# Performance work log

Hardware: AMD Instinct MI355X
Metric: run time of the kernel (lower is better)

Reference implementation:

```python
import jax, jax.numpy as jnp
import numpy as np

N_MIRNAS = 60000
N_DISEASES = 40000
N_NODES = N_MIRNAS + N_DISEASES
D = 64          # embedding_dim
L = 2           # n_layers
R = 8           # num_relations (hardcoded in module)
B = 4           # num_bases (hardcoded in module)
E = 2_000_000   # total edges


def setup_inputs() -> dict:
    key = jax.random.key(0)
    ks = jax.random.split(key, 7)
    node_embeddings = jax.random.normal(ks[0], (N_NODES, D), jnp.float32) * 0.1
    basis = jax.random.normal(ks[1], (L, B, D, D), jnp.float32) * 0.05   # basis_weights per layer
    coeff = jax.random.normal(ks[2], (L, R, B), jnp.float32) * 0.2       # relation coefficients
    self_w = jax.random.normal(ks[3], (L, D, D), jnp.float32) * 0.05     # self-loop linear (no bias)
    bias = jnp.zeros((L, D), jnp.float32)
    edge_index = jax.random.randint(ks[4], (2, E), 0, N_NODES, dtype=jnp.int32)
    edge_type = jax.random.randint(ks[5], (E,), 0, R, dtype=jnp.int32)
    return dict(node_embeddings=node_embeddings, basis=basis, coeff=coeff,
                self_w=self_w, bias=bias, edge_index=edge_index, edge_type=edge_type)


def _rgcn_layer(x, basis, coeff, self_w, bias, edge_index, edge_type):
    # weight_r = sum_b coeff[r,b] * basis[b]  (same as torch.einsum('rb,bio->rio'))
    n = x.shape[0]
    W = jnp.einsum('rb,bio->rio', coeff, basis)            # [R, D, D]
    # transform all nodes under every relation once, then gather per edge:
    # equivalent to per-relation mask -> gather -> mm -> index_add in the original
    h = jnp.einsum('ni,rio->rno', x, W)                    # [R, N, D]
    msgs = h[edge_type, edge_index[0]]                     # [E, D] = x[src] @ W[edge_type]
    agg = jax.ops.segment_sum(msgs, edge_index[1], num_segments=n)  # index_add_ scatter
    out = x @ self_w + agg + bias                          # self-loop + messages + bias
    # dropout is identity in eval mode; module applies ReLU last
    return jax.nn.relu(out)


def reference(node_embeddings, basis, coeff, self_w, bias, edge_index, edge_type):
    x = node_embeddings
    for l in range(L):
        x = _rgcn_layer(x, basis[l], coeff[l], self_w[l], bias[l], edge_index, edge_type)
    return x[:N_MIRNAS], x[N_MIRNAS:]
```

## Files before the change

kernel.cpp:

```cpp
#include <hip/hip_runtime.h>
#include <hip/hip_bf16.h>

#define DD 64
#define EPB 8192
#define WPAD 72

typedef unsigned int u32;
typedef __attribute__((ext_vector_type(8))) short bf16x8;
typedef __attribute__((ext_vector_type(8))) unsigned short u16x8;
typedef __attribute__((ext_vector_type(4))) float f32x4;

__device__ __forceinline__ float bf2f(unsigned short u) {
  union { u32 i; float f; } c;
  c.i = ((u32)u) << 16;
  return c.f;
}
__device__ __forceinline__ unsigned short f2bf(float f) {
  __hip_bfloat16 h = __float2bfloat16(f);
  return *reinterpret_cast<unsigned short*>(&h);
}


__global__ __launch_bounds__(256) void zero_u32_kernel(u32* __restrict__ p, int n) {
  int i = blockIdx.x * 256 + threadIdx.x;
  if (i < n) p[i] = 0u;
}

__global__ __launch_bounds__(256) void coarse_hist_kernel(
    const int* __restrict__ edst, u32* __restrict__ ccnt,
    int E, int sh_bin, int nbins) {
  __shared__ u32 lh[256];
  const int t = threadIdx.x;
  for (int j = t; j < nbins; j += 256) lh[j] = 0u;
  __syncthreads();
  for (int e = blockIdx.x * 256 + t; e < E; e += gridDim.x * 256)
    atomicAdd(&lh[edst[e] >> sh_bin], 1u);
  __syncthreads();
  for (int j = t; j < nbins; j += 256) {
    u32 c = lh[j];
    if (c) atomicAdd(&ccnt[j], c);
  }
}

__global__ __launch_bounds__(256) void coarse_scan_kernel(
    const u32* __restrict__ ccnt, u32* __restrict__ bin_base,
    u32* __restrict__ bin_cursor, int nbins, int E) {
  __shared__ u32 s[256];
  const int t = threadIdx.x;
  u32 v = (t < nbins) ? ccnt[t] : 0u;
  s[t] = v;
  __syncthreads();
  for (int off = 1; off < 256; off <<= 1) {
    u32 x = (t >= off) ? s[t - off] : 0u;
    __syncthreads();
    s[t] += x;
    __syncthreads();
  }
  if (t < nbins) {
    u32 ex = s[t] - v;
    bin_base[t] = ex;
    bin_cursor[t] = ex;
  }
  if (t == 0) bin_base[nbins] = (u32)E;
}

__global__ __launch_bounds__(256) void binscatter_kernel(
    const int* __restrict__ esrc, const int* __restrict__ edst,
    const int* __restrict__ et, u32* __restrict__ bin_cursor,
    u32* __restrict__ tmp, int E, int sh_bin, int sh, int nbins) {
  __shared__ u32 lhist[256];
  __shared__ u32 lbase[256];
  const int t = threadIdx.x;
  const int base = blockIdx.x * EPB;
  for (int j = t; j < nbins; j += 256) lhist[j] = 0u;
  __syncthreads();
  u32 br[32];
#pragma unroll
  for (int k = 0; k < 32; ++k) {
    int e = base + k * 256 + t;
    if (e < E) {
      int bn = edst[e] >> sh_bin;
      u32 r = atomicAdd(&lhist[bn], 1u);
      br[k] = ((u32)bn << 13) | r;
    }
  }
  __syncthreads();
  for (int j = t; j < nbins; j += 256) {
    u32 c = lhist[j];
    lbase[j] = c ? atomicAdd(&bin_cursor[j], c) : 0u;
  }
  __syncthreads();
  const u32 wmask = (1u << sh_bin) - 1u;
#pragma unroll
  for (int k = 0; k < 32; ++k) {
    int e = base + k * 256 + t;
    if (e < E) {
      u32 bn = br[k] >> 13, r = br[k] & 0x1FFFu;
      u32 pos = lbase[bn] + r;
      u32 dlow = (u32)edst[e] & wmask;
      tmp[pos] = (u32)esrc[e] | ((u32)et[e] << sh) | (dlow << (sh + 3));
    }
  }
}

__global__ __launch_bounds__(1024) void finescatter_kernel(
    const u32* __restrict__ tmp, const u32* __restrict__ bin_base,
    u32* __restrict__ row_ptr, u32* __restrict__ packed,
    int N, int E, int sh_bin, int sh) {
  __shared__ u32 dcnt[1024];
  __shared__ u32 s[1024];
  const int t = threadIdx.x;
  const int b = blockIdx.x;
  const u32 beg = bin_base[b], end = bin_base[b + 1];
  const int W  = 1 << sh_bin;
  const int d0 = b << sh_bin;
  const int dsh = sh + 3;
  const u32 smask = (1u << sh) - 1u;

  if (t < W) dcnt[t] = 0u;
  __syncthreads();
  for (u32 e = beg + t; e < end; e += 1024)
    atomicAdd(&dcnt[tmp[e] >> dsh], 1u);
  __syncthreads();
  u32 v = (t < W) ? dcnt[t] : 0u;
  s[t] = v;
  __syncthreads();
  for (int off = 1; off < 1024; off <<= 1) {
    u32 x = (t >= off) ? s[t - off] : 0u;
    __syncthreads();
    s[t] += x;
    __syncthreads();
  }
  const u32 ex = s[t] - v;
  if (t < W) {
    int d = d0 + t;
    if (d < N) row_ptr[d] = beg + ex;
    dcnt[t] = beg + ex;
  }
  if (b == 0 && t == 0) row_ptr[N] = (u32)E;
  __syncthreads();
  for (u32 e = beg + t; e < end; e += 1024) {
    u32 p = tmp[e];
    u32 pos = atomicAdd(&dcnt[p >> dsh], 1u);
    u32 src = p & smask;
    u32 ty  = (p >> sh) & 7u;
    packed[pos] = ty * (u32)N + src;
  }
}


__global__ __launch_bounds__(256) void compute_wt_kernel(
    const float* __restrict__ basis, const float* __restrict__ coeff,
    const float* __restrict__ self_w, unsigned short* __restrict__ Wt16,
    int R, int Bn) {
  int idx = blockIdx.x * 256 + threadIdx.x;
  int total = (R + 1) * DD * DD;
  if (idx >= total) return;
  int m = idx >> 12;
  int k = (idx >> 6) & 63;
  int o = idx & 63;
  float acc = 0.f;
  if (m == R) {
    acc = self_w[k * DD + o];
  } else {
    for (int b = 0; b < Bn; ++b)
      acc += coeff[m * Bn + b] * basis[((size_t)b * DD + k) * DD + o];
  }
  Wt16[((size_t)m * DD + o) * DD + k] = f2bf(acc);
}

__global__ __launch_bounds__(256) void transform_h_kernel(
    const float* __restrict__ x, const unsigned short* __restrict__ Wt16,
    unsigned short* __restrict__ h16, int N, int R) {
  __shared__ unsigned short Ws[2][64 * WPAD];
  const int t    = threadIdx.x;
  const int w    = t >> 6;
  const int lane = t & 63;
  const int l16  = lane & 15;
  const int kg   = lane >> 4;
  const int node = blockIdx.x * DD + w * 16 + l16;
  const bool ok  = (node < N);

  bf16x8 Xfrag[2];
  {
    const float* xp = x + (size_t)(ok ? node : 0) * DD + kg * 8;
#pragma unroll
    for (int kc = 0; kc < 2; ++kc) {
      float4 v0 = ok ? *reinterpret_cast<const float4*>(xp + kc * 32)
                     : make_float4(0.f, 0.f, 0.f, 0.f);
      float4 v1 = ok ? *reinterpret_cast<const float4*>(xp + kc * 32 + 4)
                     : make_float4(0.f, 0.f, 0.f, 0.f);
      bf16x8 a;
      a[0] = (short)f2bf(v0.x); a[1] = (short)f2bf(v0.y);
      a[2] = (short)f2bf(v0.z); a[3] = (short)f2bf(v0.w);
      a[4] = (short)f2bf(v1.x); a[5] = (short)f2bf(v1.y);
      a[6] = (short)f2bf(v1.z); a[7] = (short)f2bf(v1.w);
      Xfrag[kc] = a;
    }
  }

  {
#pragma unroll
    for (int i = 0; i < 2; ++i) {
      int q = t + (i << 8);
      int row = q >> 3, c8 = (q & 7) << 3;
      u16x8 v = *reinterpret_cast<const u16x8*>(Wt16 + row * DD + c8);
      *reinterpret_cast<u16x8*>(&Ws[0][row * WPAD + c8]) = v;
    }
  }
  __syncthreads();

  for (int m = 0; m <= R; ++m) {
    const int cur = m & 1;
    if (m < R) {
      const unsigned short* wb = Wt16 + ((size_t)(m + 1) << 12);
#pragma unroll
      for (int i = 0; i < 2; ++i) {
        int q = t + (i << 8);
        int row = q >> 3, c8 = (q & 7) << 3;
        u16x8 v = *reinterpret_cast<const u16x8*>(wb + row * DD + c8);
        *reinterpret_cast<u16x8*>(&Ws[cur ^ 1][row * WPAD + c8]) = v;
      }
    }

    unsigned short* hp = h16 + (((size_t)m * N + node) << 6);
#pragma unroll
    for (int t4 = 0; t4 < 4; ++t4) {
      const unsigned short* ap = &Ws[cur][(t4 * 16 + l16) * WPAD + kg * 8];
      bf16x8 A0 = *reinterpret_cast<const bf16x8*>(ap);
      bf16x8 A1 = *reinterpret_cast<const bf16x8*>(ap + 32);
      f32x4 acc;
      acc[0] = 0.f; acc[1] = 0.f; acc[2] = 0.f; acc[3] = 0.f;
      acc = __builtin_amdgcn_mfma_f32_16x16x32_bf16(A0, Xfrag[0], acc, 0, 0, 0);
      acc = __builtin_amdgcn_mfma_f32_16x16x32_bf16(A1, Xfrag[1], acc, 0, 0, 0);
      if (ok) {
        ushort4 o4;
        o4.x = f2bf(acc[0]); o4.y = f2bf(acc[1]);
        o4.z = f2bf(acc[2]); o4.w = f2bf(acc[3]);
        *reinterpret_cast<ushort4*>(hp + t4 * 16 + kg * 4) = o4;
      }
    }
    __syncthreads();
  }
}

__global__ __launch_bounds__(256) void aggregate_out_kernel(
    const u32* __restrict__ packed, const u32* __restrict__ row_ptr,
    const unsigned short* __restrict__ h16, const float* __restrict__ bias_l,
    float* __restrict__ out, int N, int R) {
  const int wid  = (blockIdx.x * 256 + threadIdx.x) >> 6;
  const int lane = threadIdx.x & 63;
  if (wid >= N) return;
  const int g  = lane >> 3;
  const int l8 = lane & 7;
  const u32 beg = row_ptr[wid], end = row_ptr[wid + 1];

  float s[8];
  if (g == 0) {
    u16x8 v = *reinterpret_cast<const u16x8*>(
        h16 + (((size_t)R * N + wid) << 6) + l8 * 8);
#pragma unroll
    for (int j = 0; j < 8; ++j) s[j] = bf2f((unsigned short)v[j]);
  } else {
#pragma unroll
    for (int j = 0; j < 8; ++j) s[j] = 0.f;
  }

  const u32 cnt = end - beg;
  u32 e = beg;
  const u32 end16 = beg + (cnt & ~15u);
  for (; e < end16; e += 16) {
    u32 r0 = packed[e + g];
    u32 r1 = packed[e + 8 + g];
    u16x8 v0 = *reinterpret_cast<const u16x8*>(h16 + ((size_t)r0 << 6) + l8 * 8);
    u16x8 v1 = *reinterpret_cast<const u16x8*>(h16 + ((size_t)r1 << 6) + l8 * 8);
#pragma unroll
    for (int j = 0; j < 8; ++j)
      s[j] += bf2f((unsigned short)v0[j]) + bf2f((unsigned short)v1[j]);
  }
  if (e + 8 <= end) {
    u32 r0 = packed[e + g];
    u16x8 v0 = *reinterpret_cast<const u16x8*>(h16 + ((size_t)r0 << 6) + l8 * 8);
#pragma unroll
    for (int j = 0; j < 8; ++j) s[j] += bf2f((unsigned short)v0[j]);
    e += 8;
  }
  if (e < end) {
    u32 eg = e + g;
    if (eg < end) {
      u32 r0 = packed[eg];
      u16x8 v0 = *reinterpret_cast<const u16x8*>(h16 + ((size_t)r0 << 6) + l8 * 8);
#pragma unroll
      for (int j = 0; j < 8; ++j) s[j] += bf2f((unsigned short)v0[j]);
    }
  }

#pragma unroll
  for (int j = 0; j < 8; ++j) {
    s[j] += __shfl_xor(s[j], 8);
    s[j] += __shfl_xor(s[j], 16);
    s[j] += __shfl_xor(s[j], 32);
  }

  if (g == 0) {
    const float* bp = bias_l + l8 * 8;
    float4 o0, o1;
    o0.x = fmaxf(s[0] + bp[0], 0.f);
    o0.y = fmaxf(s[1] + bp[1], 0.f);
    o0.z = fmaxf(s[2] + bp[2], 0.f);
    o0.w = fmaxf(s[3] + bp[3], 0.f);
    o1.x = fmaxf(s[4] + bp[4], 0.f);
    o1.y = fmaxf(s[5] + bp[5], 0.f);
    o1.z = fmaxf(s[6] + bp[6], 0.f);
    o1.w = fmaxf(s[7] + bp[7], 0.f);
    float* op = out + ((size_t)wid << 6) + l8 * 8;
    *reinterpret_cast<float4*>(op) = o0;
    *reinterpret_cast<float4*>(op + 4) = o1;
  }
}

extern "C" void kernel_launch(void* const* d_in, const int* in_sizes, int n_in,
                              void* d_out, int out_size, void* d_ws, size_t ws_size,
                              hipStream_t stream) {
  const float* x0     = (const float*)d_in[0];
  const float* basis  = (const float*)d_in[1];
  const float* coeff  = (const float*)d_in[2];
  const float* self_w = (const float*)d_in[3];
  const float* bias   = (const float*)d_in[4];
  const int*   eidx   = (const int*)d_in[5];
  const int*   etyp   = (const int*)d_in[6];

  const int N  = in_sizes[0] / DD;
  const int L  = in_sizes[4] / DD;
  const int Bn = in_sizes[1] / (L * DD * DD);
  const int R  = in_sizes[2] / (L * Bn);
  const int E  = in_sizes[6];

  int sh = 0;
  while ((1 << sh) < N) ++sh;
  int sh_bin = 0;
  while ((((N - 1) >> sh_bin) + 1) > 256) ++sh_bin;
  const int nbins = ((N - 1) >> sh_bin) + 1;

  const int* esrc = eidx;
  const int* edst = eidx + E;

  u32* row_ptr = (u32*)d_ws;
  u32* packed  = row_ptr + N + 1;
  size_t u32B  = (((size_t)N + 1 + E) * 4 + 15) / 16 * 16;
  unsigned short* Wt16 = (unsigned short*)((char*)d_ws + u32B);
  size_t wtB   = (u32B + (size_t)(R + 1) * DD * DD * 2 + 15) / 16 * 16;
  float* A     = (float*)((char*)d_ws + wtB);
  unsigned short* h16 = (unsigned short*)(A + (size_t)N * DD);
  u32* ccnt       = (u32*)h16;
  u32* bin_base   = ccnt + 256;
  u32* bin_cursor = bin_base + 257;
  u32* tmp        = bin_cursor + 256 + 3;

  const int nb_bs  = (E + EPB - 1) / EPB;
  const int nb_agg = (int)(((size_t)N * 64 + 255) / 256);
  const int nb_x   = (N + DD - 1) / DD;
  const int nb_wt  = ((R + 1) * DD * DD + 255) / 256;

  zero_u32_kernel<<<1, 256, 0, stream>>>(ccnt, nbins);
  coarse_hist_kernel<<<1024, 256, 0, stream>>>(edst, ccnt, E, sh_bin, nbins);
  coarse_scan_kernel<<<1, 256, 0, stream>>>(ccnt, bin_base, bin_cursor, nbins, E);
  binscatter_kernel<<<nb_bs, 256, 0, stream>>>(
      esrc, edst, etyp, bin_cursor, tmp, E, sh_bin, sh, nbins);
  finescatter_kernel<<<nbins, 1024, 0, stream>>>(
      tmp, bin_base, row_ptr, packed, N, E, sh_bin, sh);

  for (int l = 0; l < L; ++l) {
    const float* xin = (l == 0) ? x0 : A;
    float* outf      = (l == L - 1) ? (float*)d_out : A;

    compute_wt_kernel<<<nb_wt, 256, 0, stream>>>(
        basis + (size_t)l * Bn * DD * DD, coeff + (size_t)l * R * Bn,
        self_w + (size_t)l * DD * DD, Wt16, R, Bn);

    transform_h_kernel<<<nb_x, 256, 0, stream>>>(xin, Wt16, h16, N, R);

    aggregate_out_kernel<<<nb_agg, 256, 0, stream>>>(
        packed, row_ptr, h16, bias + (size_t)l * DD, outf, N, R);
  }
}
```

Baseline: 330.0 us.

## Store intermediate layer activations in bf16 and permute h feature layout for wide stores

The intermediate activation between layers is now written by the aggregation kernel as bf16 rather than fp32 and read directly as MFMA fragments by the next transform, removing a conversion and halving that buffer's traffic. The transform kernel also keeps all four MFMA accumulators and writes each row's outputs as two 16-byte stores in a permuted feature order instead of four 8-byte stores. The aggregation epilogue undoes that permutation when adding bias and writing output. The change adds one extra bf16 rounding of the hidden activations, which the transform already applied before MFMA.

```diff
diff --git a/kernel.cpp b/kernel.cpp
--- a/kernel.cpp
+++ b/kernel.cpp
@@ -170,7 +170,8 @@
 }
 
 __global__ __launch_bounds__(256) void transform_h_kernel(
-    const float* __restrict__ x, const unsigned short* __restrict__ Wt16,
+    const void* __restrict__ xin, int x_is_bf16,
+    const unsigned short* __restrict__ Wt16,
     unsigned short* __restrict__ h16, int N, int R) {
   __shared__ unsigned short Ws[2][64 * WPAD];
   const int t    = threadIdx.x;
@@ -182,8 +183,21 @@
   const bool ok  = (node < N);
 
   bf16x8 Xfrag[2];
-  {
-    const float* xp = x + (size_t)(ok ? node : 0) * DD + kg * 8;
+  if (x_is_bf16) {
+    const unsigned short* xp =
+        (const unsigned short*)xin + ((size_t)(ok ? node : 0) << 6) + kg * 8;
+#pragma unroll
+    for (int kc = 0; kc < 2; ++kc) {
+      u16x8 v;
+      if (ok) v = *reinterpret_cast<const u16x8*>(xp + kc * 32);
+      else {
+#pragma unroll
+        for (int j = 0; j < 8; ++j) v[j] = 0;
+      }
+      Xfrag[kc] = *reinterpret_cast<bf16x8*>(&v);
+    }
+  } else {
+    const float* xp = (const float*)xin + (size_t)(ok ? node : 0) * DD + kg * 8;
 #pragma unroll
     for (int kc = 0; kc < 2; ++kc) {
       float4 v0 = ok ? *reinterpret_cast<const float4*>(xp + kc * 32)
@@ -223,22 +237,28 @@
       }
     }
 
-    unsigned short* hp = h16 + (((size_t)m * N + node) << 6);
+    f32x4 acc[4];
 #pragma unroll
     for (int t4 = 0; t4 < 4; ++t4) {
       const unsigned short* ap = &Ws[cur][(t4 * 16 + l16) * WPAD + kg * 8];
       bf16x8 A0 = *reinterpret_cast<const bf16x8*>(ap);
       bf16x8 A1 = *reinterpret_cast<const bf16x8*>(ap + 32);
-      f32x4 acc;
-      acc[0] = 0.f; acc[1] = 0.f; acc[2] = 0.f; acc[3] = 0.f;
-      acc = __builtin_amdgcn_mfma_f32_16x16x32_bf16(A0, Xfrag[0], acc, 0, 0, 0);
-      acc = __builtin_amdgcn_mfma_f32_16x16x32_bf16(A1, Xfrag[1], acc, 0, 0, 0);
-      if (ok) {
-        ushort4 o4;
-        o4.x = f2bf(acc[0]); o4.y = f2bf(acc[1]);
-        o4.z = f2bf(acc[2]); o4.w = f2bf(acc[3]);
-        *reinterpret_cast<ushort4*>(hp + t4 * 16 + kg * 4) = o4;
+      acc[t4][0] = 0.f; acc[t4][1] = 0.f; acc[t4][2] = 0.f; acc[t4][3] = 0.f;
+      acc[t4] = __builtin_amdgcn_mfma_f32_16x16x32_bf16(A0, Xfrag[0], acc[t4], 0, 0, 0);
+      acc[t4] = __builtin_amdgcn_mfma_f32_16x16x32_bf16(A1, Xfrag[1], acc[t4], 0, 0, 0);
+    }
+    if (ok) {
+      unsigned short* hp = h16 + (((size_t)m * N + node) << 6) + kg * 16;
+      u16x8 o0, o1;
+#pragma unroll
+      for (int j = 0; j < 4; ++j) {
+        o0[j]     = f2bf(acc[0][j]);
+        o0[4 + j] = f2bf(acc[1][j]);
+        o1[j]     = f2bf(acc[2][j]);
+        o1[4 + j] = f2bf(acc[3][j]);
       }
+      *reinterpret_cast<u16x8*>(hp) = o0;
+      *reinterpret_cast<u16x8*>(hp + 8) = o1;
     }
     __syncthreads();
   }
@@ -247,7 +267,7 @@
 __global__ __launch_bounds__(256) void aggregate_out_kernel(
     const u32* __restrict__ packed, const u32* __restrict__ row_ptr,
     const unsigned short* __restrict__ h16, const float* __restrict__ bias_l,
-    float* __restrict__ out, int N, int R) {
+    void* __restrict__ outv, int out_is_bf16, int N, int R) {
   const int wid  = (blockIdx.x * 256 + threadIdx.x) >> 6;
   const int lane = threadIdx.x & 63;
   if (wid >= N) return;
@@ -303,19 +323,28 @@
   }
 
   if (g == 0) {
-    const float* bp = bias_l + l8 * 8;
-    float4 o0, o1;
-    o0.x = fmaxf(s[0] + bp[0], 0.f);
-    o0.y = fmaxf(s[1] + bp[1], 0.f);
-    o0.z = fmaxf(s[2] + bp[2], 0.f);
-    o0.w = fmaxf(s[3] + bp[3], 0.f);
-    o1.x = fmaxf(s[4] + bp[4], 0.f);
-    o1.y = fmaxf(s[5] + bp[5], 0.f);
-    o1.z = fmaxf(s[6] + bp[6], 0.f);
-    o1.w = fmaxf(s[7] + bp[7], 0.f);
-    float* op = out + ((size_t)wid << 6) + l8 * 8;
-    *reinterpret_cast<float4*>(op) = o0;
-    *reinterpret_cast<float4*>(op + 4) = o1;
+    const int f_lo = ((l8 & 1) << 5) | ((l8 >> 1) << 2);
+    const int f_hi = f_lo + 16;
+    const float4 blo = *reinterpret_cast<const float4*>(bias_l + f_lo);
+    const float4 bhi = *reinterpret_cast<const float4*>(bias_l + f_hi);
+    float r0 = fmaxf(s[0] + blo.x, 0.f), r1 = fmaxf(s[1] + blo.y, 0.f);
+    float r2 = fmaxf(s[2] + blo.z, 0.f), r3 = fmaxf(s[3] + blo.w, 0.f);
+    float r4 = fmaxf(s[4] + bhi.x, 0.f), r5 = fmaxf(s[5] + bhi.y, 0.f);
+    float r6 = fmaxf(s[6] + bhi.z, 0.f), r7 = fmaxf(s[7] + bhi.w, 0.f);
+    if (out_is_bf16) {
+      unsigned short* op = (unsigned short*)outv + ((size_t)wid << 6);
+      ushort4 a, b;
+      a.x = f2bf(r0); a.y = f2bf(r1); a.z = f2bf(r2); a.w = f2bf(r3);
+      b.x = f2bf(r4); b.y = f2bf(r5); b.z = f2bf(r6); b.w = f2bf(r7);
+      *reinterpret_cast<ushort4*>(op + f_lo) = a;
+      *reinterpret_cast<ushort4*>(op + f_hi) = b;
+    } else {
+      float* op = (float*)outv + ((size_t)wid << 6);
+      float4 a = make_float4(r0, r1, r2, r3);
+      float4 b = make_float4(r4, r5, r6, r7);
+      *reinterpret_cast<float4*>(op + f_lo) = a;
+      *reinterpret_cast<float4*>(op + f_hi) = b;
+    }
   }
 }
 
@@ -350,8 +379,8 @@
   size_t u32B  = (((size_t)N + 1 + E) * 4 + 15) / 16 * 16;
   unsigned short* Wt16 = (unsigned short*)((char*)d_ws + u32B);
   size_t wtB   = (u32B + (size_t)(R + 1) * DD * DD * 2 + 15) / 16 * 16;
-  float* A     = (float*)((char*)d_ws + wtB);
-  unsigned short* h16 = (unsigned short*)(A + (size_t)N * DD);
+  unsigned short* A16 = (unsigned short*)((char*)d_ws + wtB);
+  unsigned short* h16 = A16 + ((size_t)N << 6);
   u32* ccnt       = (u32*)h16;
   u32* bin_base   = ccnt + 256;
   u32* bin_cursor = bin_base + 257;
@@ -371,16 +400,22 @@
       tmp, bin_base, row_ptr, packed, N, E, sh_bin, sh);
 
   for (int l = 0; l < L; ++l) {
-    const float* xin = (l == 0) ? x0 : A;
-    float* outf      = (l == L - 1) ? (float*)d_out : A;
-
     compute_wt_kernel<<<nb_wt, 256, 0, stream>>>(
         basis + (size_t)l * Bn * DD * DD, coeff + (size_t)l * R * Bn,
         self_w + (size_t)l * DD * DD, Wt16, R, Bn);
 
-    transform_h_kernel<<<nb_x, 256, 0, stream>>>(xin, Wt16, h16, N, R);
-
-    aggregate_out_kernel<<<nb_agg, 256, 0, stream>>>(
-        packed, row_ptr, h16, bias + (size_t)l * DD, outf, N, R);
-  }
-}
+    if (l == 0) {
+      transform_h_kernel<<<nb_x, 256, 0, stream>>>(x0, 0, Wt16, h16, N, R);
+    } else {
+      transform_h_kernel<<<nb_x, 256, 0, stream>>>(A16, 1, Wt16, h16, N, R);
+    }
+
+    if (l == L - 1) {
+      aggregate_out_kernel<<<nb_agg, 256, 0, stream>>>(
+          packed, row_ptr, h16, bias + (size_t)l * DD, d_out, 0, N, R);
+    } else {
+      aggregate_out_kernel<<<nb_agg, 256, 0, stream>>>(
+          packed, row_ptr, h16, bias + (size_t)l * DD, A16, 1, N, R);
+    }
+  }
+}
```

After: 301.8 us, median of 2. -8.6%, faster.
